# Optimization experiments

Measured on AMD Instinct MI355X. Metric: run time of the kernel, lower is better.

The kernel has to match this reference:

```python
import jax, jax.numpy as jnp
import numpy as np

B, T, E = 16, 512, 768
N_ANN = 32                      # mentions per passage
N_ENT = B * N_ANN               # 512 flat entities, each 2E wide
P = B * N_ANN * (N_ANN - 1)     # 15872 ordered pairs
H = 512                          # MLP hidden size (head_args layer_sizes)
ENTITY_DIM = 256                 # relation MLP output = 2*entity_dim
D4 = 4 * E                       # relation_input width


def setup_inputs() -> dict:
    key = jax.random.key(0)
    ks = jax.random.split(key, 14)
    inp = {
        "x": jax.random.normal(ks[0], (B, T, E), dtype=jnp.float32),
        "src_tokens": jax.random.randint(ks[1], (B, T), 0, 32000),
        "mask_annotation": jax.random.randint(ks[2], (B, T), 0, 2),
        "all_annotations": jax.random.randint(ks[3], (B, 2 * N_ANN), 0, T),
        "n_annotations": N_ANN,
        "relation_entity_indices_left": jax.random.randint(ks[4], (P,), 0, N_ENT),
        "relation_entity_indices_right": jax.random.randint(ks[5], (P,), 0, N_ENT),
        # relation MLP: Linear(4E,H) -> ReLU -> Linear(H, 2*entity_dim)
        "W1": jax.random.normal(ks[6], (D4, H), dtype=jnp.float32) / np.sqrt(D4),
        "b1": jnp.zeros((H,), dtype=jnp.float32),
        "W2": jax.random.normal(ks[7], (H, 2 * ENTITY_DIM), dtype=jnp.float32) / np.sqrt(H),
        "b2": jnp.zeros((2 * ENTITY_DIM,), dtype=jnp.float32),
        # score MLP: Linear(4E,H) -> ReLU -> Linear(H, 1)
        "Ws1": jax.random.normal(ks[8], (D4, H), dtype=jnp.float32) / np.sqrt(D4),
        "bs1": jnp.zeros((H,), dtype=jnp.float32),
        "Ws2": jax.random.normal(ks[9], (H, 1), dtype=jnp.float32) / np.sqrt(H),
        "bs2": jnp.zeros((1,), dtype=jnp.float32),
    }
    return inp


def reference(x, src_tokens, mask_annotation, all_annotations, n_annotations,
              relation_entity_indices_left, relation_entity_indices_right,
              W1, b1, W2, b2, Ws1, bs1, Ws2, bs2):
    batch_size, _, enc_dim = x.shape
    # idx_repeated: each batch row repeated 2*n_annotations times
    idx_rep = jnp.repeat(jnp.arange(batch_size), 2 * n_annotations)
    ann_flat = all_annotations.reshape(-1)
    # gather annotation tokens -> [B*2n, E] -> pairwise concat [B*n, 2E]
    ent_tokens = x[idx_rep, ann_flat]
    entity_representation = ent_tokens.reshape(-1, 2 * enc_dim)
    left = entity_representation[relation_entity_indices_left]
    right = entity_representation[relation_entity_indices_right]
    relation_input = jnp.concatenate((left, right), axis=-1)  # [P, 4E]
    h_rel = jax.nn.relu(relation_input @ W1 + b1)
    relation_representation = h_rel @ W2 + b2                 # [P, 2*entity_dim]
    h_sc = jax.nn.relu(relation_input @ Ws1 + bs1)
    relation_score = jnp.abs((h_sc @ Ws2 + bs2).squeeze(-1))  # [P]
    return entity_representation, relation_representation, relation_score
```

## Files before the change

kernel.cpp:

```cpp
#include <hip/hip_runtime.h>

typedef unsigned short u16;
typedef __attribute__((ext_vector_type(8))) short short8;
typedef __attribute__((ext_vector_type(4))) float floatx4;

#define P_PAIRS 15872
#define E_DIM   768
#define D2      1536
#define OUT_ENT   (512*1536)
#define OUT_REL   (15872*512)

__device__ __forceinline__ u16 f2bf(float f){
    union { float f; unsigned u; } v; v.f = f;
    unsigned r = v.u + 0x7fffu + ((v.u >> 16) & 1u);
    return (u16)(r >> 16);
}
__device__ __forceinline__ unsigned pack2(float a, float b){
    return (unsigned)f2bf(a) | ((unsigned)f2bf(b) << 16);
}
__device__ __forceinline__ void async_ld16(const void* g, void* lds_base){
    __builtin_amdgcn_global_load_lds(
        (const __attribute__((address_space(1))) unsigned*)g,
        (__attribute__((address_space(3))) unsigned*)lds_base, 16, 0, 0);
}

__global__ __launch_bounds__(256)
void prep_k(const float* __restrict__ W1, const float* __restrict__ Ws1,
            const float* __restrict__ W2, const float* __restrict__ x,
            const int* __restrict__ ann,
            u16* __restrict__ W1T, u16* __restrict__ Ws1T, u16* __restrict__ W2T,
            float* __restrict__ entF, u16* __restrict__ entB) {
    const int bid = blockIdx.x;
    const int t = threadIdx.x;
    if (bid < 3328) {
        __shared__ float tile[32][33];
        const float* src; u16* dst; int R, C, b;
        if (bid < 1536)      { src = W1;  dst = W1T;  R = 3072; C = 512; b = bid; }
        else if (bid < 3072) { src = Ws1; dst = Ws1T; R = 3072; C = 512; b = bid - 1536; }
        else                 { src = W2;  dst = W2T;  R = 512;  C = 512; b = bid - 3072; }
        const int bx = (b & 15) * 32;
        const int by = (b >> 4) * 32;
        const int tx = t & 31, ty = t >> 5;
#pragma unroll
        for (int i = 0; i < 32; i += 8)
            tile[ty + i][tx] = src[(size_t)(by + ty + i) * C + bx + tx];
        __syncthreads();
#pragma unroll
        for (int i = 0; i < 32; i += 8)
            dst[(size_t)(bx + ty + i) * R + by + tx] = f2bf(tile[tx][ty + i]);
    } else {
        const int e = bid - 3328;
#pragma unroll
        for (int pass = 0; pass < 2; pass++) {
            const int c = t + pass * 256;
            if (c >= 384) break;
            const int half = c / 192;
            const int tok = ann[e * 2 + half];
            const int b = e >> 5;
            const float4 v = ((const float4*)(x + (size_t)(b * 512 + tok) * E_DIM))[c % 192];
            ((float4*)(entF + (size_t)e * D2))[c] = v;
            uint2 o; o.x = pack2(v.x, v.y); o.y = pack2(v.z, v.w);
            ((uint2*)(entB + (size_t)e * D2))[c] = o;
        }
    }
}

__global__ __launch_bounds__(256)
void gemm_uv(const u16* __restrict__ Ent, const u16* __restrict__ W1T,
             const u16* __restrict__ Ws1T, float* __restrict__ UV) {
    __shared__ __align__(16) u16 As[64 * 32];
    __shared__ __align__(16) u16 Bs[64 * 32];
    const int t = threadIdx.x;
    const int bid = blockIdx.x;
    const int m0 = (bid & 7) * 64;
    const int n0g = (bid >> 3) * 64;
    const int g = n0g >> 9;
    const int n0 = n0g & 511;
    const u16* WT = (g < 2) ? W1T : Ws1T;
    const int koff = (g & 1) * D2;

    const int wave = t >> 6, lane = t & 63;
    const int wm = (wave >> 1) * 32, wn = (wave & 1) * 32;
    const int l15 = lane & 15, quad = lane >> 4;
    const int srow = t >> 2;
    const int sk = (t & 3) * 8;

    const u16* gA = Ent + (size_t)(m0 + srow) * D2 + sk;
    const u16* gB = WT + (size_t)(n0 + srow) * 3072 + koff + sk;
    u16* lA = As + wave * 512;
    u16* lB = Bs + wave * 512;

    floatx4 acc[2][2] = {};
    for (int k0 = 0; k0 < D2; k0 += 32) {
        __syncthreads();
        async_ld16(gA + k0, lA);
        async_ld16(gB + k0, lB);
        __syncthreads();
        short8 af[2], bf[2];
#pragma unroll
        for (int i = 0; i < 2; i++) {
            af[i] = *(const short8*)(As + (wm + i * 16 + l15) * 32 + quad * 8);
            bf[i] = *(const short8*)(Bs + (wn + i * 16 + l15) * 32 + quad * 8);
        }
#pragma unroll
        for (int i = 0; i < 2; i++)
#pragma unroll
            for (int j = 0; j < 2; j++)
                acc[i][j] = __builtin_amdgcn_mfma_f32_16x16x32_bf16(af[i], bf[j], acc[i][j], 0, 0, 0);
    }
    float* outg = UV + (size_t)g * 262144;
#pragma unroll
    for (int j = 0; j < 2; j++) {
        const int col = n0 + wn + j * 16 + l15;
#pragma unroll
        for (int i = 0; i < 2; i++) {
            const int rowb = m0 + wm + i * 16 + quad * 4;
#pragma unroll
            for (int r = 0; r < 4; r++)
                outg[(size_t)(rowb + r) * 512 + col] = acc[i][j][r];
        }
    }
}

__global__ __launch_bounds__(256)
void rel_score_k(const float* __restrict__ UV, const int* __restrict__ left,
                 const int* __restrict__ right, const float* __restrict__ b1,
                 const float* __restrict__ bs1, const float* __restrict__ Ws2,
                 const float* __restrict__ bs2, const u16* __restrict__ W2T,
                 const float* __restrict__ b2, float* __restrict__ rel,
                 float* __restrict__ score) {
    const int bid = blockIdx.x;
    const int t = threadIdx.x;
    const int wave = t >> 6, lane = t & 63;

    if (bid < 496) {
        __shared__ __align__(16) u16 As[128 * 32];
        __shared__ __align__(16) u16 Bs[128 * 32];
        const int m0 = (bid >> 2) * 128;
        const int n0 = (bid & 3) * 128;
        const int wm = (wave >> 1) * 64, wn = (wave & 1) * 64;
        const int l15 = lane & 15, quad = lane >> 4;

        const int arow = t >> 1;
        const int koff16 = (t & 1) * 16;
        const int li = left[m0 + arow], ri = right[m0 + arow];
        const float4* Up = (const float4*)(UV + (size_t)li * 512 + koff16);
        const float4* Vp = (const float4*)(UV + 262144 + (size_t)ri * 512 + koff16);
        const float4* B1 = (const float4*)(b1 + koff16);
        const int brow = t >> 2;
        const int bk = (t & 3) * 8;
        const u16* gB0 = W2T + (size_t)(n0 + brow) * 512 + bk;
        const u16* gB1 = W2T + (size_t)(n0 + 64 + brow) * 512 + bk;
        u16* lB0 = Bs + wave * 512;
        u16* lB1 = Bs + 2048 + wave * 512;
        uint4* aDst = (uint4*)(As + t * 16);

        floatx4 acc[4][4] = {};
        for (int k0 = 0; k0 < 512; k0 += 32) {
            float4 uu[4], vv[4], bb[4];
            const int kq = k0 >> 2;
#pragma unroll
            for (int j = 0; j < 4; j++) {
                uu[j] = Up[kq + j]; vv[j] = Vp[kq + j]; bb[j] = B1[kq + j];
            }
            __syncthreads();
            async_ld16(gB0 + k0, lB0);
            async_ld16(gB1 + k0, lB1);
            uint4 h0, h1;
            {
                float4 h;
                h.x = fmaxf(uu[0].x + vv[0].x + bb[0].x, 0.f);
                h.y = fmaxf(uu[0].y + vv[0].y + bb[0].y, 0.f);
                h.z = fmaxf(uu[0].z + vv[0].z + bb[0].z, 0.f);
                h.w = fmaxf(uu[0].w + vv[0].w + bb[0].w, 0.f);
                h0.x = pack2(h.x, h.y); h0.y = pack2(h.z, h.w);
                h.x = fmaxf(uu[1].x + vv[1].x + bb[1].x, 0.f);
                h.y = fmaxf(uu[1].y + vv[1].y + bb[1].y, 0.f);
                h.z = fmaxf(uu[1].z + vv[1].z + bb[1].z, 0.f);
                h.w = fmaxf(uu[1].w + vv[1].w + bb[1].w, 0.f);
                h0.z = pack2(h.x, h.y); h0.w = pack2(h.z, h.w);
                h.x = fmaxf(uu[2].x + vv[2].x + bb[2].x, 0.f);
                h.y = fmaxf(uu[2].y + vv[2].y + bb[2].y, 0.f);
                h.z = fmaxf(uu[2].z + vv[2].z + bb[2].z, 0.f);
                h.w = fmaxf(uu[2].w + vv[2].w + bb[2].w, 0.f);
                h1.x = pack2(h.x, h.y); h1.y = pack2(h.z, h.w);
                h.x = fmaxf(uu[3].x + vv[3].x + bb[3].x, 0.f);
                h.y = fmaxf(uu[3].y + vv[3].y + bb[3].y, 0.f);
                h.z = fmaxf(uu[3].z + vv[3].z + bb[3].z, 0.f);
                h.w = fmaxf(uu[3].w + vv[3].w + bb[3].w, 0.f);
                h1.z = pack2(h.x, h.y); h1.w = pack2(h.z, h.w);
            }
            aDst[0] = h0; aDst[1] = h1;
            __syncthreads();
            short8 af[4], bf[4];
#pragma unroll
            for (int i = 0; i < 4; i++) {
                af[i] = *(const short8*)(As + (wm + i * 16 + l15) * 32 + quad * 8);
                bf[i] = *(const short8*)(Bs + (wn + i * 16 + l15) * 32 + quad * 8);
            }
#pragma unroll
            for (int i = 0; i < 4; i++)
#pragma unroll
                for (int j = 0; j < 4; j++)
                    acc[i][j] = __builtin_amdgcn_mfma_f32_16x16x32_bf16(af[i], bf[j], acc[i][j], 0, 0, 0);
        }
#pragma unroll
        for (int j = 0; j < 4; j++) {
            const int col = n0 + wn + j * 16 + l15;
            const float bias = b2[col];
#pragma unroll
            for (int i = 0; i < 4; i++) {
                const int rowb = m0 + wm + i * 16 + quad * 4;
#pragma unroll
                for (int r = 0; r < 4; r++)
                    rel[(size_t)(rowb + r) * 512 + col] = acc[i][j][r] + bias;
            }
        }
    } else {
        const int pid0 = (bid - 496) * 32 + wave * 8;
        const float4* Wsp = (const float4*)(Ws2 + lane * 8);
        const float4* Bsp = (const float4*)(bs1 + lane * 8);
        const float4 w0 = Wsp[0], w1 = Wsp[1];
        const float4 s0 = Bsp[0], s1 = Bsp[1];
        const float bias = bs2[0];
#pragma unroll
        for (int it = 0; it < 8; it++) {
            const int p = pid0 + it;
            const int l = left[p], r = right[p];
            const float4* us = (const float4*)(UV + 2 * 262144 + (size_t)l * 512 + lane * 8);
            const float4* vs = (const float4*)(UV + 3 * 262144 + (size_t)r * 512 + lane * 8);
            const float4 a0 = us[0], a1 = us[1];
            const float4 c0 = vs[0], c1 = vs[1];
            float acc;
            acc  = fmaxf(a0.x + c0.x + s0.x, 0.f) * w0.x;
            acc += fmaxf(a0.y + c0.y + s0.y, 0.f) * w0.y;
            acc += fmaxf(a0.z + c0.z + s0.z, 0.f) * w0.z;
            acc += fmaxf(a0.w + c0.w + s0.w, 0.f) * w0.w;
            acc += fmaxf(a1.x + c1.x + s1.x, 0.f) * w1.x;
            acc += fmaxf(a1.y + c1.y + s1.y, 0.f) * w1.y;
            acc += fmaxf(a1.z + c1.z + s1.z, 0.f) * w1.z;
            acc += fmaxf(a1.w + c1.w + s1.w, 0.f) * w1.w;
#pragma unroll
            for (int off = 32; off; off >>= 1) acc += __shfl_down(acc, off, 64);
            if (lane == 0) score[p] = fabsf(acc + bias);
        }
    }
}

extern "C" void kernel_launch(void* const* d_in, const int* in_sizes, int n_in,
                              void* d_out, int out_size, void* d_ws, size_t ws_size,
                              hipStream_t stream) {
    const float* x   = (const float*)d_in[0];
    const int* ann   = (const int*)d_in[3];
    const int* left  = (const int*)d_in[5];
    const int* right = (const int*)d_in[6];
    const float* W1  = (const float*)d_in[7];
    const float* b1  = (const float*)d_in[8];
    const float* W2  = (const float*)d_in[9];
    const float* b2  = (const float*)d_in[10];
    const float* Ws1 = (const float*)d_in[11];
    const float* bs1 = (const float*)d_in[12];
    const float* Ws2 = (const float*)d_in[13];
    const float* bs2 = (const float*)d_in[14];

    float* out = (float*)d_out;
    float* entF = out;
    float* rel  = out + OUT_ENT;
    float* sco  = out + OUT_ENT + OUT_REL;

    u16* W1T  = (u16*)d_ws;
    u16* Ws1T = W1T + 512 * 3072;
    u16* W2T  = Ws1T + 512 * 3072;
    u16* EntB = W2T + 512 * 512;
    float* UV = (float*)(EntB + 512 * 1536);

    prep_k<<<3840, 256, 0, stream>>>(W1, Ws1, W2, x, ann, W1T, Ws1T, W2T, entF, EntB);
    gemm_uv<<<256, 256, 0, stream>>>(EntB, W1T, Ws1T, UV);
    rel_score_k<<<992, 256, 0, stream>>>(UV, left, right, b1, bs1, Ws2, bs2, W2T, b2, rel, sco);
}
```

Measured before the change: 165.5 us.

## Double-buffer LDS tiles with XOR swizzle and fold hidden biases into UV GEMM

Measured after the change: 160.9 us (median of 2 runs). -2.8%, faster.

```diff
diff --git a/kernel.cpp b/kernel.cpp
--- a/kernel.cpp
+++ b/kernel.cpp
@@ -67,9 +67,10 @@
 
 __global__ __launch_bounds__(256)
 void gemm_uv(const u16* __restrict__ Ent, const u16* __restrict__ W1T,
-             const u16* __restrict__ Ws1T, float* __restrict__ UV) {
-    __shared__ __align__(16) u16 As[64 * 32];
-    __shared__ __align__(16) u16 Bs[64 * 32];
+             const u16* __restrict__ Ws1T, const float* __restrict__ b1,
+             const float* __restrict__ bs1, float* __restrict__ UV) {
+    __shared__ __align__(16) u16 As[2][64 * 64];
+    __shared__ __align__(16) u16 Bs[2][64 * 64];
     const int t = threadIdx.x;
     const int bid = blockIdx.x;
     const int m0 = (bid & 7) * 64;
@@ -82,50 +83,68 @@
     const int wave = t >> 6, lane = t & 63;
     const int wm = (wave >> 1) * 32, wn = (wave & 1) * 32;
     const int l15 = lane & 15, quad = lane >> 4;
-    const int srow = t >> 2;
-    const int sk = (t & 3) * 8;
-
-    const u16* gA = Ent + (size_t)(m0 + srow) * D2 + sk;
-    const u16* gB = WT + (size_t)(n0 + srow) * 3072 + koff + sk;
-    u16* lA = As + wave * 512;
-    u16* lB = Bs + wave * 512;
+
+    const int lr = lane >> 3;
+    const int k8 = (lane & 7) ^ lr;
+    const int rowA0 = wave * 16 + lr;
+    const u16* gA0 = Ent + (size_t)(m0 + rowA0) * D2 + k8 * 8;
+    const u16* gA1 = Ent + (size_t)(m0 + rowA0 + 8) * D2 + k8 * 8;
+    const u16* gB0 = WT + (size_t)(n0 + rowA0) * 3072 + koff + k8 * 8;
+    const u16* gB1 = WT + (size_t)(n0 + rowA0 + 8) * 3072 + koff + k8 * 8;
+    const int lofs0 = wave * 1024, lofs1 = wave * 1024 + 512;
 
     floatx4 acc[2][2] = {};
-    for (int k0 = 0; k0 < D2; k0 += 32) {
+    async_ld16(gA0, As[0] + lofs0);
+    async_ld16(gA1, As[0] + lofs1);
+    async_ld16(gB0, Bs[0] + lofs0);
+    async_ld16(gB1, Bs[0] + lofs1);
+    for (int i = 0; i < 24; i++) {
+        const int cur = i & 1;
         __syncthreads();
-        async_ld16(gA + k0, lA);
-        async_ld16(gB + k0, lB);
-        __syncthreads();
-        short8 af[2], bf[2];
-#pragma unroll
-        for (int i = 0; i < 2; i++) {
-            af[i] = *(const short8*)(As + (wm + i * 16 + l15) * 32 + quad * 8);
-            bf[i] = *(const short8*)(Bs + (wn + i * 16 + l15) * 32 + quad * 8);
-        }
-#pragma unroll
-        for (int i = 0; i < 2; i++)
-#pragma unroll
-            for (int j = 0; j < 2; j++)
-                acc[i][j] = __builtin_amdgcn_mfma_f32_16x16x32_bf16(af[i], bf[j], acc[i][j], 0, 0, 0);
+        if (i + 1 < 24) {
+            const int k1 = (i + 1) * 64;
+            async_ld16(gA0 + k1, As[cur ^ 1] + lofs0);
+            async_ld16(gA1 + k1, As[cur ^ 1] + lofs1);
+            async_ld16(gB0 + k1, Bs[cur ^ 1] + lofs0);
+            async_ld16(gB1 + k1, Bs[cur ^ 1] + lofs1);
+        }
+        const u16* Ac = As[cur];
+        const u16* Bc = Bs[cur];
+#pragma unroll
+        for (int kk = 0; kk < 2; kk++) {
+            short8 af[2], bf[2];
+#pragma unroll
+            for (int i2 = 0; i2 < 2; i2++) {
+                const int ra = wm + i2 * 16 + l15;
+                af[i2] = *(const short8*)(Ac + (ra * 8 + ((quad + kk * 4) ^ (ra & 7))) * 8);
+                const int rb = wn + i2 * 16 + l15;
+                bf[i2] = *(const short8*)(Bc + (rb * 8 + ((quad + kk * 4) ^ (rb & 7))) * 8);
+            }
+#pragma unroll
+            for (int i2 = 0; i2 < 2; i2++)
+#pragma unroll
+                for (int j2 = 0; j2 < 2; j2++)
+                    acc[i2][j2] = __builtin_amdgcn_mfma_f32_16x16x32_bf16(af[i2], bf[j2], acc[i2][j2], 0, 0, 0);
+        }
     }
     float* outg = UV + (size_t)g * 262144;
 #pragma unroll
     for (int j = 0; j < 2; j++) {
         const int col = n0 + wn + j * 16 + l15;
+        const float bias = (g == 0) ? b1[col] : (g == 2) ? bs1[col] : 0.f;
 #pragma unroll
         for (int i = 0; i < 2; i++) {
             const int rowb = m0 + wm + i * 16 + quad * 4;
 #pragma unroll
             for (int r = 0; r < 4; r++)
-                outg[(size_t)(rowb + r) * 512 + col] = acc[i][j][r];
+                outg[(size_t)(rowb + r) * 512 + col] = acc[i][j][r] + bias;
         }
     }
 }
 
 __global__ __launch_bounds__(256)
 void rel_score_k(const float* __restrict__ UV, const int* __restrict__ left,
-                 const int* __restrict__ right, const float* __restrict__ b1,
-                 const float* __restrict__ bs1, const float* __restrict__ Ws2,
+                 const int* __restrict__ right, const float* __restrict__ Ws2,
                  const float* __restrict__ bs2, const u16* __restrict__ W2T,
                  const float* __restrict__ b2, float* __restrict__ rel,
                  float* __restrict__ score) {
@@ -134,75 +153,87 @@
     const int wave = t >> 6, lane = t & 63;
 
     if (bid < 496) {
-        __shared__ __align__(16) u16 As[128 * 32];
-        __shared__ __align__(16) u16 Bs[128 * 32];
+        __shared__ __align__(16) u16 As[2][128 * 32];
+        __shared__ __align__(16) u16 Bs[2][128 * 32];
         const int m0 = (bid >> 2) * 128;
         const int n0 = (bid & 3) * 128;
         const int wm = (wave >> 1) * 64, wn = (wave & 1) * 64;
         const int l15 = lane & 15, quad = lane >> 4;
 
         const int arow = t >> 1;
-        const int koff16 = (t & 1) * 16;
+        const int kh = t & 1;
         const int li = left[m0 + arow], ri = right[m0 + arow];
-        const float4* Up = (const float4*)(UV + (size_t)li * 512 + koff16);
-        const float4* Vp = (const float4*)(UV + 262144 + (size_t)ri * 512 + koff16);
-        const float4* B1 = (const float4*)(b1 + koff16);
-        const int brow = t >> 2;
-        const int bk = (t & 3) * 8;
-        const u16* gB0 = W2T + (size_t)(n0 + brow) * 512 + bk;
-        const u16* gB1 = W2T + (size_t)(n0 + 64 + brow) * 512 + bk;
-        u16* lB0 = Bs + wave * 512;
-        u16* lB1 = Bs + 2048 + wave * 512;
-        uint4* aDst = (uint4*)(As + t * 16);
+        const float4* Up = (const float4*)(UV + (size_t)li * 512 + kh * 16);
+        const float4* Vp = (const float4*)(UV + 262144 + (size_t)ri * 512 + kh * 16);
+        const int sA0 = arow * 4 + ((kh * 2) ^ (arow & 3));
+        const int sA1 = arow * 4 + ((kh * 2 + 1) ^ (arow & 3));
+        const int browl = lane >> 2;
+        const int bk8 = (lane & 3) ^ (browl & 3);
+        const u16* gB0 = W2T + (size_t)(n0 + wave * 32 + browl) * 512 + bk8 * 8;
+        const u16* gB1 = W2T + (size_t)(n0 + wave * 32 + 16 + browl) * 512 + bk8 * 8;
+        const int lofs0 = wave * 1024, lofs1 = wave * 1024 + 512;
 
         floatx4 acc[4][4] = {};
-        for (int k0 = 0; k0 < 512; k0 += 32) {
-            float4 uu[4], vv[4], bb[4];
-            const int kq = k0 >> 2;
-#pragma unroll
-            for (int j = 0; j < 4; j++) {
-                uu[j] = Up[kq + j]; vv[j] = Vp[kq + j]; bb[j] = B1[kq + j];
+        float4 uu[4], vv[4];
+#pragma unroll
+        for (int j = 0; j < 4; j++) { uu[j] = Up[j]; vv[j] = Vp[j]; }
+        async_ld16(gB0, Bs[0] + lofs0);
+        async_ld16(gB1, Bs[0] + lofs1);
+        {
+            uint4 h0, h1;
+            h0.x = pack2(fmaxf(uu[0].x + vv[0].x, 0.f), fmaxf(uu[0].y + vv[0].y, 0.f));
+            h0.y = pack2(fmaxf(uu[0].z + vv[0].z, 0.f), fmaxf(uu[0].w + vv[0].w, 0.f));
+            h0.z = pack2(fmaxf(uu[1].x + vv[1].x, 0.f), fmaxf(uu[1].y + vv[1].y, 0.f));
+            h0.w = pack2(fmaxf(uu[1].z + vv[1].z, 0.f), fmaxf(uu[1].w + vv[1].w, 0.f));
+            h1.x = pack2(fmaxf(uu[2].x + vv[2].x, 0.f), fmaxf(uu[2].y + vv[2].y, 0.f));
+            h1.y = pack2(fmaxf(uu[2].z + vv[2].z, 0.f), fmaxf(uu[2].w + vv[2].w, 0.f));
+            h1.z = pack2(fmaxf(uu[3].x + vv[3].x, 0.f), fmaxf(uu[3].y + vv[3].y, 0.f));
+            h1.w = pack2(fmaxf(uu[3].z + vv[3].z, 0.f), fmaxf(uu[3].w + vv[3].w, 0.f));
+            *(uint4*)(As[0] + sA0 * 8) = h0;
+            *(uint4*)(As[0] + sA1 * 8) = h1;
+        }
+#pragma unroll
+        for (int j = 0; j < 4; j++) { uu[j] = Up[8 + j]; vv[j] = Vp[8 + j]; }
+
+        for (int i = 0; i < 16; i++) {
+            const int cur = i & 1;
+            __syncthreads();
+            if (i + 1 < 16) {
+                const int k1 = (i + 1) * 32;
+                async_ld16(gB0 + k1, Bs[cur ^ 1] + lofs0);
+                async_ld16(gB1 + k1, Bs[cur ^ 1] + lofs1);
+                uint4 h0, h1;
+                h0.x = pack2(fmaxf(uu[0].x + vv[0].x, 0.f), fmaxf(uu[0].y + vv[0].y, 0.f));
+                h0.y = pack2(fmaxf(uu[0].z + vv[0].z, 0.f), fmaxf(uu[0].w + vv[0].w, 0.f));
+                h0.z = pack2(fmaxf(uu[1].x + vv[1].x, 0.f), fmaxf(uu[1].y + vv[1].y, 0.f));
+                h0.w = pack2(fmaxf(uu[1].z + vv[1].z, 0.f), fmaxf(uu[1].w + vv[1].w, 0.f));
+                h1.x = pack2(fmaxf(uu[2].x + vv[2].x, 0.f), fmaxf(uu[2].y + vv[2].y, 0.f));
+                h1.y = pack2(fmaxf(uu[2].z + vv[2].z, 0.f), fmaxf(uu[2].w + vv[2].w, 0.f));
+                h1.z = pack2(fmaxf(uu[3].x + vv[3].x, 0.f), fmaxf(uu[3].y + vv[3].y, 0.f));
+                h1.w = pack2(fmaxf(uu[3].z + vv[3].z, 0.f), fmaxf(uu[3].w + vv[3].w, 0.f));
+                *(uint4*)(As[cur ^ 1] + sA0 * 8) = h0;
+                *(uint4*)(As[cur ^ 1] + sA1 * 8) = h1;
+                if (i + 2 < 16) {
+                    const int q = (i + 2) * 8;
+#pragma unroll
+                    for (int j = 0; j < 4; j++) { uu[j] = Up[q + j]; vv[j] = Vp[q + j]; }
+                }
             }
-            __syncthreads();
-            async_ld16(gB0 + k0, lB0);
-            async_ld16(gB1 + k0, lB1);
-            uint4 h0, h1;
-            {
-                float4 h;
-                h.x = fmaxf(uu[0].x + vv[0].x + bb[0].x, 0.f);
-                h.y = fmaxf(uu[0].y + vv[0].y + bb[0].y, 0.f);
-                h.z = fmaxf(uu[0].z + vv[0].z + bb[0].z, 0.f);
-                h.w = fmaxf(uu[0].w + vv[0].w + bb[0].w, 0.f);
-                h0.x = pack2(h.x, h.y); h0.y = pack2(h.z, h.w);
-                h.x = fmaxf(uu[1].x + vv[1].x + bb[1].x, 0.f);
-                h.y = fmaxf(uu[1].y + vv[1].y + bb[1].y, 0.f);
-                h.z = fmaxf(uu[1].z + vv[1].z + bb[1].z, 0.f);
-                h.w = fmaxf(uu[1].w + vv[1].w + bb[1].w, 0.f);
-                h0.z = pack2(h.x, h.y); h0.w = pack2(h.z, h.w);
-                h.x = fmaxf(uu[2].x + vv[2].x + bb[2].x, 0.f);
-                h.y = fmaxf(uu[2].y + vv[2].y + bb[2].y, 0.f);
-                h.z = fmaxf(uu[2].z + vv[2].z + bb[2].z, 0.f);
-                h.w = fmaxf(uu[2].w + vv[2].w + bb[2].w, 0.f);
-                h1.x = pack2(h.x, h.y); h1.y = pack2(h.z, h.w);
-                h.x = fmaxf(uu[3].x + vv[3].x + bb[3].x, 0.f);
-                h.y = fmaxf(uu[3].y + vv[3].y + bb[3].y, 0.f);
-                h.z = fmaxf(uu[3].z + vv[3].z + bb[3].z, 0.f);
-                h.w = fmaxf(uu[3].w + vv[3].w + bb[3].w, 0.f);
-                h1.z = pack2(h.x, h.y); h1.w = pack2(h.z, h.w);
+            const u16* Ac = As[cur];
+            const u16* Bc = Bs[cur];
+            short8 af[4], bf[4];
+#pragma unroll
+            for (int i2 = 0; i2 < 4; i2++) {
+                const int ra = wm + i2 * 16 + l15;
+                af[i2] = *(const short8*)(Ac + (ra * 4 + (quad ^ (ra & 3))) * 8);
+                const int rb = wn + i2 * 16 + l15;
+                bf[i2] = *(const short8*)(Bc + (rb * 4 + (quad ^ (rb & 3))) * 8);
             }
-            aDst[0] = h0; aDst[1] = h1;
-            __syncthreads();
-            short8 af[4], bf[4];
-#pragma unroll
-            for (int i = 0; i < 4; i++) {
-                af[i] = *(const short8*)(As + (wm + i * 16 + l15) * 32 + quad * 8);
-                bf[i] = *(const short8*)(Bs + (wn + i * 16 + l15) * 32 + quad * 8);
-            }
-#pragma unroll
-            for (int i = 0; i < 4; i++)
-#pragma unroll
-                for (int j = 0; j < 4; j++)
-                    acc[i][j] = __builtin_amdgcn_mfma_f32_16x16x32_bf16(af[i], bf[j], acc[i][j], 0, 0, 0);
+#pragma unroll
+            for (int i2 = 0; i2 < 4; i2++)
+#pragma unroll
+                for (int j2 = 0; j2 < 4; j2++)
+                    acc[i2][j2] = __builtin_amdgcn_mfma_f32_16x16x32_bf16(af[i2], bf[j2], acc[i2][j2], 0, 0, 0);
         }
 #pragma unroll
         for (int j = 0; j < 4; j++) {
@@ -219,9 +250,7 @@
     } else {
         const int pid0 = (bid - 496) * 32 + wave * 8;
         const float4* Wsp = (const float4*)(Ws2 + lane * 8);
-        const float4* Bsp = (const float4*)(bs1 + lane * 8);
         const float4 w0 = Wsp[0], w1 = Wsp[1];
-        const float4 s0 = Bsp[0], s1 = Bsp[1];
         const float bias = bs2[0];
 #pragma unroll
         for (int it = 0; it < 8; it++) {
@@ -232,14 +261,14 @@
             const float4 a0 = us[0], a1 = us[1];
             const float4 c0 = vs[0], c1 = vs[1];
             float acc;
-            acc  = fmaxf(a0.x + c0.x + s0.x, 0.f) * w0.x;
-            acc += fmaxf(a0.y + c0.y + s0.y, 0.f) * w0.y;
-            acc += fmaxf(a0.z + c0.z + s0.z, 0.f) * w0.z;
-            acc += fmaxf(a0.w + c0.w + s0.w, 0.f) * w0.w;
-            acc += fmaxf(a1.x + c1.x + s1.x, 0.f) * w1.x;
-            acc += fmaxf(a1.y + c1.y + s1.y, 0.f) * w1.y;
-            acc += fmaxf(a1.z + c1.z + s1.z, 0.f) * w1.z;
-            acc += fmaxf(a1.w + c1.w + s1.w, 0.f) * w1.w;
+            acc  = fmaxf(a0.x + c0.x, 0.f) * w0.x;
+            acc += fmaxf(a0.y + c0.y, 0.f) * w0.y;
+            acc += fmaxf(a0.z + c0.z, 0.f) * w0.z;
+            acc += fmaxf(a0.w + c0.w, 0.f) * w0.w;
+            acc += fmaxf(a1.x + c1.x, 0.f) * w1.x;
+            acc += fmaxf(a1.y + c1.y, 0.f) * w1.y;
+            acc += fmaxf(a1.z + c1.z, 0.f) * w1.z;
+            acc += fmaxf(a1.w + c1.w, 0.f) * w1.w;
 #pragma unroll
             for (int off = 32; off; off >>= 1) acc += __shfl_down(acc, off, 64);
             if (lane == 0) score[p] = fabsf(acc + bias);
@@ -275,6 +304,6 @@
     float* UV = (float*)(EntB + 512 * 1536);
 
     prep_k<<<3840, 256, 0, stream>>>(W1, Ws1, W2, x, ann, W1T, Ws1T, W2T, entF, EntB);
-    gemm_uv<<<256, 256, 0, stream>>>(EntB, W1T, Ws1T, UV);
-    rel_score_k<<<992, 256, 0, stream>>>(UV, left, right, b1, bs1, Ws2, bs2, W2T, b2, rel, sco);
-}
+    gemm_uv<<<256, 256, 0, stream>>>(EntB, W1T, Ws1T, b1, bs1, UV);
+    rel_score_k<<<992, 256, 0, stream>>>(UV, left, right, Ws2, bs2, W2T, b2, rel, sco);
+}
```
